# Kernel tuning notes

Measured on AMD Instinct MI355X. Metric: run time of the kernel, lower is better.

## Reference

```python
import jax, jax.numpy as jnp
import numpy as np

B, S, D = 4, 2048, 1024

def setup_inputs() -> dict:
    key = jax.random.key(0)
    kx, kq, kk, kv = jax.random.split(key, 4)
    scale = 0.02
    return {
        'x': jax.random.normal(kx, (B, S, D), dtype=jnp.float32),
        'wq': jax.random.normal(kq, (D, D), dtype=jnp.float32) * scale,
        'wk': jax.random.normal(kk, (D, D), dtype=jnp.float32) * scale,
        'wv': jax.random.normal(kv, (D, D), dtype=jnp.float32) * scale,
    }

def reference(x, wq, wk, wv):
    # QKV projections (no bias): nn.Linear applies x @ W^T; here wq is already [d_in, d_out]
    q = jnp.einsum('bsd,de->bse', x, wq)
    k = jnp.einsum('bsd,de->bse', x, wk)
    v = jnp.einsum('bsd,de->bse', x, wv)
    d_k = k.shape[-1]
    scores = jnp.einsum('bqd,bkd->bqk', q, k) / jnp.sqrt(jnp.float32(d_k))
    s = x.shape[1]
    causal = jnp.tril(jnp.ones((s, s), dtype=bool))  # True = keep
    scores = jnp.where(causal[None, :, :], scores, -jnp.inf)
    attn = jax.nn.softmax(scores, axis=-1)
    # dropout p=0.0 -> identity
    return jnp.einsum('bqk,bkd->bqd', attn, v)
```

## Files before the change

### kernel.cpp

```cpp
#include <hip/hip_runtime.h>
#include <hip/hip_bf16.h>


typedef __attribute__((ext_vector_type(8))) short bf16x8;
typedef __attribute__((ext_vector_type(4))) float f32x4;

#define GLOAD_LDS16(g, l)                                                     \
    __builtin_amdgcn_global_load_lds(                                         \
        (const __attribute__((address_space(1))) void*)(g),                   \
        (__attribute__((address_space(3))) void*)(l), 16, 0, 0)

__device__ __forceinline__ short f2bf(float f) {
    union { float f; unsigned u; } v; v.f = f;
    unsigned r = v.u + 0x7FFFu + ((v.u >> 16) & 1u);
    return (short)(r >> 16);
}
__device__ __forceinline__ float bf2f(short h) {
    union { unsigned u; float f; } v;
    v.u = ((unsigned)(unsigned short)h) << 16;
    return v.f;
}

__global__ __launch_bounds__(256) void convall(
    const float* __restrict__ x, const float* __restrict__ wq,
    const float* __restrict__ wk, short* __restrict__ xb,
    short* __restrict__ wqb, short* __restrict__ wkb) {
    int i = blockIdx.x * 256 + threadIdx.x;
#pragma unroll
    for (int s = 0; s < 5; ++s) {
        int v = i + s * 524288;
        const float* src;
        short* dst;
        int off;
        if (v < 2097152)      { src = x;  dst = xb;  off = v; }
        else if (v < 2359296) { src = wq; dst = wqb; off = v - 2097152; }
        else                  { src = wk; dst = wkb; off = v - 2359296; }
        float4 w = ((const float4*)src)[off];
        short4 o;
        o.x = f2bf(w.x); o.y = f2bf(w.y); o.z = f2bf(w.z); o.w = f2bf(w.w);
        ((short4*)dst)[off] = o;
    }
}

__global__ __launch_bounds__(256) void wtrans(const float* __restrict__ W,
                                              short* __restrict__ O) {
    int n0 = blockIdx.x * 64, k0 = blockIdx.y * 64;
    __shared__ float tile[64][65];
    int t = threadIdx.x;
#pragma unroll
    for (int i = 0; i < 16; ++i) {
        int idx = t + i * 256;
        int r = idx >> 6, c = idx & 63;
        tile[r][c] = W[(size_t)(k0 + r) * 1024 + n0 + c];
    }
    __syncthreads();
#pragma unroll
    for (int i = 0; i < 16; ++i) {
        int idx = t + i * 256;
        int r = idx >> 6, c = idx & 63;
        O[(size_t)(n0 + r) * 1024 + k0 + c] = f2bf(tile[c][r]);
    }
}

template <int MODE>
__global__ __launch_bounds__(256, 2) void gemm128(
    const short* __restrict__ A0, int lda0, long long sA,
    const short* __restrict__ B0, int ldb0, long long sB,
    void* __restrict__ C0, float scale,
    const short* __restrict__ Av, const short* __restrict__ Bv,
    short* __restrict__ Cv) {

    int m0, n0, z = 0, lda = lda0, ldb = ldb0;
    const short* Ab;
    const short* Bb;
    bool isVT = false;

    if (MODE == 2) {
        int i = blockIdx.x;
        int j = i & 255;
        int mt = (i < 256) ? (15 - (j >> 5)) : (j >> 5);
        z = (j >> 3) & 3;
        m0 = mt * 128;
        n0 = (j & 7) * 128;
        Ab = A0 + (size_t)z * sA;
        Bb = B0 + (size_t)z * sB;
    } else {
        const int nblk = gridDim.x;
        const int raw = blockIdx.x;
        int bid = (raw & 7) * (nblk >> 3) + (raw >> 3);
        if (MODE == 5) {
            m0 = (bid >> 3) * 128;
            n0 = (bid & 7) * 128;
            Ab = A0; Bb = B0;
        } else {
            if (bid < 544) {
                z = bid / 136;
                int f = bid - z * 136;
                int mt = (int)((sqrtf(8.f * f + 1.f) - 1.f) * 0.5f);
                if (mt * (mt + 1) / 2 > f) --mt;
                if ((mt + 1) * (mt + 2) / 2 <= f) ++mt;
                int nt_ = f - mt * (mt + 1) / 2;
                m0 = mt * 128; n0 = nt_ * 128;
                Ab = A0 + (size_t)z * sA;
                Bb = B0 + (size_t)z * sB;
            } else {
                isVT = true;
                int v = bid - 544;
                m0 = (v >> 6) * 128;
                n0 = (v & 63) * 128;
                Ab = Av; Bb = Bv; lda = 1024; ldb = 1024;
            }
        }
    }

    const int tid = threadIdx.x;
    const int lane = tid & 63;
    const int wid = tid >> 6;
    const int wm = wid >> 1, wn = wid & 1;

    __shared__ __align__(16) short As[2][8192];
    __shared__ __align__(16) short Bs[2][8192];

    f32x4 acc[4][4] = {};

    const int Kend = (MODE == 2) ? (m0 + 128) : 1024;
    const int nt = Kend >> 6;

    const int srow = tid >> 3;
    const int sl = (tid & 7) ^ (srow & 7);
    const short* Agp = Ab + (size_t)(m0 + srow) * lda + sl * 8;
    const short* Bgp = Bb + (size_t)(n0 + srow) * ldb + sl * 8;

#define SA(kt, bf)                                                            \
    do {                                                                      \
        const int _k = (kt) << 6;                                             \
        GLOAD_LDS16(Agp + _k,                     &As[bf][tid * 8]);          \
        GLOAD_LDS16(Agp + _k + (size_t)32 * lda,  &As[bf][2048 + tid * 8]);   \
        GLOAD_LDS16(Agp + _k + (size_t)64 * lda,  &As[bf][4096 + tid * 8]);   \
        GLOAD_LDS16(Agp + _k + (size_t)96 * lda,  &As[bf][6144 + tid * 8]);   \
    } while (0)
#define SB(kt, bf)                                                            \
    do {                                                                      \
        const int _k = (kt) << 6;                                             \
        GLOAD_LDS16(Bgp + _k,                     &Bs[bf][tid * 8]);          \
        GLOAD_LDS16(Bgp + _k + (size_t)32 * ldb,  &Bs[bf][2048 + tid * 8]);   \
        GLOAD_LDS16(Bgp + _k + (size_t)64 * ldb,  &Bs[bf][4096 + tid * 8]);   \
        GLOAD_LDS16(Bgp + _k + (size_t)96 * ldb,  &Bs[bf][6144 + tid * 8]);   \
    } while (0)

    const int r = lane & 15;
    const int g = lane >> 4;

#define LDA4(dst, bf, kk)                                                     \
    _Pragma("unroll") for (int q = 0; q < 4; ++q) {                           \
        const int rr = wm * 64 + q * 16 + r;                                  \
        dst[q] = *(const bf16x8*)&As[bf][rr * 64 +                            \
                                         ((((kk)*4 + g) ^ (rr & 7))) * 8];    \
    }
#define LDB4(dst, bf, kk)                                                     \
    _Pragma("unroll") for (int q = 0; q < 4; ++q) {                           \
        const int rb = wn * 64 + q * 16 + r;                                  \
        dst[q] = *(const bf16x8*)&Bs[bf][rb * 64 +                            \
                                         ((((kk)*4 + g) ^ (rb & 7))) * 8];    \
    }
#define LGKM(n)                                                               \
    asm volatile("s_waitcnt lgkmcnt(" #n ")" ::: "memory");                   \
    __builtin_amdgcn_sched_barrier(0)
#define VM0() asm volatile("s_waitcnt vmcnt(0)" ::: "memory")
#define BAR() __builtin_amdgcn_s_barrier()
#define MF(ar, br)                                                            \
    _Pragma("unroll") for (int mi = 0; mi < 4; ++mi)                          \
        _Pragma("unroll") for (int ni = 0; ni < 4; ++ni)                      \
            acc[mi][ni] = __builtin_amdgcn_mfma_f32_16x16x32_bf16(            \
                ar[mi], br[ni], acc[mi][ni], 0, 0, 0);

    SA(0, 0); SB(0, 0);
    VM0();
    BAR();

    int buf = 0;
    for (int t = 0; t < nt - 1; ++t) {
        const int nb = buf ^ 1;
        SA(t + 1, nb); SB(t + 1, nb);
        bf16x8 a0[4], b0[4], a1[4], b1[4];
        LDA4(a0, buf, 0); LDB4(b0, buf, 0);
        __builtin_amdgcn_sched_barrier(0);
        LDA4(a1, buf, 1); LDB4(b1, buf, 1);
        LGKM(8);
        MF(a0, b0);
        LGKM(0);
        MF(a1, b1);
        VM0();
        BAR();
        buf = nb;
    }
    {
        bf16x8 a0[4], b0[4], a1[4], b1[4];
        LDA4(a0, buf, 0); LDB4(b0, buf, 0);
        __builtin_amdgcn_sched_barrier(0);
        LDA4(a1, buf, 1); LDB4(b1, buf, 1);
        LGKM(8);
        MF(a0, b0);
        LGKM(0);
        MF(a1, b1);
    }

    const int r4 = (lane >> 4) * 4;
#pragma unroll
    for (int mi = 0; mi < 4; ++mi) {
#pragma unroll
        for (int ni = 0; ni < 4; ++ni) {
            int col = n0 + wn * 64 + ni * 16 + r;
#pragma unroll
            for (int i = 0; i < 4; ++i) {
                int rr = m0 + wm * 64 + mi * 16 + r4 + i;
                float v = acc[mi][ni][i];
                if (MODE == 5) {
                    ((short*)C0)[(size_t)rr * 1024 + col] = f2bf(v * scale);
                } else if (MODE == 1) {
                    if (isVT) {
                        Cv[(size_t)(col >> 11) * 2097152 +
                           (size_t)rr * 2048 + (col & 2047)] = f2bf(v);
                    } else if (col <= rr) {
                        ((short*)C0)[(size_t)z * 4194304 +
                                     (size_t)rr * 2048 + col] = f2bf(v);
                    }
                } else {
                    ((float*)C0)[(size_t)z * 2097152 +
                                 (size_t)rr * 1024 + col] = v;
                }
            }
        }
    }
#undef SA
#undef SB
#undef LDA4
#undef LDB4
#undef LGKM
#undef VM0
#undef BAR
#undef MF
}

__global__ __launch_bounds__(256) void softmax_wave(short* __restrict__ scores) {
    int row = (blockIdx.x << 2) + (threadIdx.x >> 6);
    int lane = threadIdx.x & 63;
    int b = row >> 11, i = row & 2047;
    short* srow = scores + ((size_t)(b << 11) + i) * 2048;
    int L = i + 1;
    int Lpad = (i | 127) + 1;

    float vals[32];
    float mx = -1e30f;
#pragma unroll
    for (int s = 0; s < 4; ++s) {
        if (s * 512 < Lpad) {
            int j0 = (s << 9) + (lane << 3);
            bf16x8 h = *(const bf16x8*)&srow[j0];
#pragma unroll
            for (int e = 0; e < 8; ++e) {
                float f = ((j0 + e) < L) ? bf2f(h[e]) : -1e30f;
                vals[s * 8 + e] = f;
                mx = fmaxf(mx, f);
            }
        }
    }
#pragma unroll
    for (int o = 32; o > 0; o >>= 1) mx = fmaxf(mx, __shfl_down(mx, o));
    mx = __shfl(mx, 0);

    float sum = 0.f;
#pragma unroll
    for (int s = 0; s < 4; ++s) {
        if (s * 512 < Lpad) {
#pragma unroll
            for (int e = 0; e < 8; ++e) {
                float ex = __expf(vals[s * 8 + e] - mx);
                vals[s * 8 + e] = ex;
                sum += ex;
            }
        }
    }
#pragma unroll
    for (int o = 32; o > 0; o >>= 1) sum += __shfl_down(sum, o);
    sum = __shfl(sum, 0);
    float rinv = 1.0f / sum;

#pragma unroll
    for (int s = 0; s < 4; ++s) {
        if (s * 512 < Lpad) {
            int j0 = (s << 9) + (lane << 3);
            bf16x8 o8;
#pragma unroll
            for (int e = 0; e < 8; ++e) o8[e] = f2bf(vals[s * 8 + e] * rinv);
            *(bf16x8*)&srow[j0] = o8;
        }
    }
}

extern "C" void kernel_launch(void* const* d_in, const int* in_sizes, int n_in,
                              void* d_out, int out_size, void* d_ws, size_t ws_size,
                              hipStream_t stream) {
    const float* x  = (const float*)d_in[0];
    const float* wq = (const float*)d_in[1];
    const float* wk = (const float*)d_in[2];
    const float* wv = (const float*)d_in[3];
    float* out = (float*)d_out;

    short* ws16 = (short*)d_ws;
    short* xb  = ws16;
    short* wqb = xb + 8388608;
    short* wkb = wqb + 1048576;
    short* wtv = wkb + 1048576;
    short* Mt  = wtv + 1048576;
    short* tb  = Mt + 1048576;
    short* vt  = tb + 8388608;
    short* scores = vt + 8388608;

    convall<<<2048, 256, 0, stream>>>(x, wq, wk, xb, wqb, wkb);
    wtrans<<<dim3(16, 16, 1), 256, 0, stream>>>(wv, wtv);
    gemm128<5><<<64, 256, 0, stream>>>(
        wkb, 1024, 0LL, wqb, 1024, 0LL, Mt, 0.03125f,
        nullptr, nullptr, nullptr);
    gemm128<5><<<512, 256, 0, stream>>>(
        xb, 1024, 0LL, Mt, 1024, 0LL, tb, 1.0f,
        nullptr, nullptr, nullptr);
    gemm128<1><<<1056, 256, 0, stream>>>(
        tb, 1024, 2097152LL, xb, 1024, 2097152LL, scores, 1.0f,
        wtv, xb, vt);
    softmax_wave<<<2048, 256, 0, stream>>>(scores);
    gemm128<2><<<512, 256, 0, stream>>>(
        scores, 2048, 4194304LL, vt, 2048, 2097152LL, out, 1.0f,
        nullptr, nullptr, nullptr);
}
```

Baseline: 164.1 us.

## Switch GEMM to triple-buffered K=32 tiles with deeper prefetch and 3 blocks/CU

```diff
diff --git a/kernel.cpp b/kernel.cpp
--- a/kernel.cpp
+++ b/kernel.cpp
@@ -63,7 +63,7 @@
 }
 
 template <int MODE>
-__global__ __launch_bounds__(256, 2) void gemm128(
+__global__ __launch_bounds__(256, 3) void gemm128(
     const short* __restrict__ A0, int lda0, long long sA,
     const short* __restrict__ B0, int ldb0, long long sB,
     void* __restrict__ C0, float scale,
@@ -118,55 +118,51 @@
     const int wid = tid >> 6;
     const int wm = wid >> 1, wn = wid & 1;
 
-    __shared__ __align__(16) short As[2][8192];
-    __shared__ __align__(16) short Bs[2][8192];
+    __shared__ __align__(16) short As[3][4096];
+    __shared__ __align__(16) short Bs[3][4096];
 
     f32x4 acc[4][4] = {};
 
     const int Kend = (MODE == 2) ? (m0 + 128) : 1024;
-    const int nt = Kend >> 6;
-
-    const int srow = tid >> 3;
-    const int sl = (tid & 7) ^ (srow & 7);
+    const int nt = Kend >> 5;
+
+    const int srow = tid >> 2;
+    const int sl = (tid & 3) ^ ((tid >> 3) & 3);
     const short* Agp = Ab + (size_t)(m0 + srow) * lda + sl * 8;
     const short* Bgp = Bb + (size_t)(n0 + srow) * ldb + sl * 8;
 
 #define SA(kt, bf)                                                            \
     do {                                                                      \
-        const int _k = (kt) << 6;                                             \
-        GLOAD_LDS16(Agp + _k,                     &As[bf][tid * 8]);          \
-        GLOAD_LDS16(Agp + _k + (size_t)32 * lda,  &As[bf][2048 + tid * 8]);   \
-        GLOAD_LDS16(Agp + _k + (size_t)64 * lda,  &As[bf][4096 + tid * 8]);   \
-        GLOAD_LDS16(Agp + _k + (size_t)96 * lda,  &As[bf][6144 + tid * 8]);   \
+        const int _k = (kt) << 5;                                             \
+        GLOAD_LDS16(Agp + _k,                    &As[bf][tid * 8]);           \
+        GLOAD_LDS16(Agp + _k + (size_t)64 * lda, &As[bf][2048 + tid * 8]);    \
     } while (0)
 #define SB(kt, bf)                                                            \
     do {                                                                      \
-        const int _k = (kt) << 6;                                             \
-        GLOAD_LDS16(Bgp + _k,                     &Bs[bf][tid * 8]);          \
-        GLOAD_LDS16(Bgp + _k + (size_t)32 * ldb,  &Bs[bf][2048 + tid * 8]);   \
-        GLOAD_LDS16(Bgp + _k + (size_t)64 * ldb,  &Bs[bf][4096 + tid * 8]);   \
-        GLOAD_LDS16(Bgp + _k + (size_t)96 * ldb,  &Bs[bf][6144 + tid * 8]);   \
+        const int _k = (kt) << 5;                                             \
+        GLOAD_LDS16(Bgp + _k,                    &Bs[bf][tid * 8]);           \
+        GLOAD_LDS16(Bgp + _k + (size_t)64 * ldb, &Bs[bf][2048 + tid * 8]);    \
     } while (0)
 
     const int r = lane & 15;
     const int g = lane >> 4;
 
-#define LDA4(dst, bf, kk)                                                     \
+#define LDA4(dst, bf)                                                         \
     _Pragma("unroll") for (int q = 0; q < 4; ++q) {                           \
         const int rr = wm * 64 + q * 16 + r;                                  \
-        dst[q] = *(const bf16x8*)&As[bf][rr * 64 +                            \
-                                         ((((kk)*4 + g) ^ (rr & 7))) * 8];    \
-    }
-#define LDB4(dst, bf, kk)                                                     \
+        dst[q] = *(const bf16x8*)&As[bf][rr * 32 +                            \
+                                         ((g ^ ((rr >> 1) & 3))) * 8];        \
+    }
+#define LDB4(dst, bf)                                                         \
     _Pragma("unroll") for (int q = 0; q < 4; ++q) {                           \
         const int rb = wn * 64 + q * 16 + r;                                  \
-        dst[q] = *(const bf16x8*)&Bs[bf][rb * 64 +                            \
-                                         ((((kk)*4 + g) ^ (rb & 7))) * 8];    \
-    }
-#define LGKM(n)                                                               \
-    asm volatile("s_waitcnt lgkmcnt(" #n ")" ::: "memory");                   \
+        dst[q] = *(const bf16x8*)&Bs[bf][rb * 32 +                            \
+                                         ((g ^ ((rb >> 1) & 3))) * 8];        \
+    }
+#define LGKM0()                                                               \
+    asm volatile("s_waitcnt lgkmcnt(0)" ::: "memory");                        \
     __builtin_amdgcn_sched_barrier(0)
-#define VM0() asm volatile("s_waitcnt vmcnt(0)" ::: "memory")
+#define VMC(n) asm volatile("s_waitcnt vmcnt(" #n ")" ::: "memory")
 #define BAR() __builtin_amdgcn_s_barrier()
 #define MF(ar, br)                                                            \
     _Pragma("unroll") for (int mi = 0; mi < 4; ++mi)                          \
@@ -175,34 +171,27 @@
                 ar[mi], br[ni], acc[mi][ni], 0, 0, 0);
 
     SA(0, 0); SB(0, 0);
-    VM0();
-    BAR();
-
-    int buf = 0;
-    for (int t = 0; t < nt - 1; ++t) {
-        const int nb = buf ^ 1;
-        SA(t + 1, nb); SB(t + 1, nb);
-        bf16x8 a0[4], b0[4], a1[4], b1[4];
-        LDA4(a0, buf, 0); LDB4(b0, buf, 0);
-        __builtin_amdgcn_sched_barrier(0);
-        LDA4(a1, buf, 1); LDB4(b1, buf, 1);
-        LGKM(8);
-        MF(a0, b0);
-        LGKM(0);
-        MF(a1, b1);
-        VM0();
+    SA(1, 1); SB(1, 1);
+
+    int bf = 0;
+    int bs = 2;
+    for (int t = 0; t < nt; ++t) {
+        bf16x8 a[4], b[4];
+        if (t + 2 < nt) {
+            SA(t + 2, bs); SB(t + 2, bs);
+            VMC(8);
+        } else if (t + 1 < nt) {
+            VMC(4);
+        } else {
+            VMC(0);
+        }
         BAR();
-        buf = nb;
-    }
-    {
-        bf16x8 a0[4], b0[4], a1[4], b1[4];
-        LDA4(a0, buf, 0); LDB4(b0, buf, 0);
-        __builtin_amdgcn_sched_barrier(0);
-        LDA4(a1, buf, 1); LDB4(b1, buf, 1);
-        LGKM(8);
-        MF(a0, b0);
-        LGKM(0);
-        MF(a1, b1);
+        LDA4(a, bf); LDB4(b, bf);
+        LGKM0();
+        MF(a, b);
+        BAR();
+        bf = (bf == 2) ? 0 : bf + 1;
+        bs = (bs == 2) ? 0 : bs + 1;
     }
 
     const int r4 = (lane >> 4) * 4;
@@ -236,8 +225,8 @@
 #undef SB
 #undef LDA4
 #undef LDB4
-#undef LGKM
-#undef VM0
+#undef LGKM0
+#undef VMC
 #undef BAR
 #undef MF
 }
```

Result: no change. 166.8 us (+1.7%).
